# Optimization experiments

Measured on AMD Instinct MI355X. Metric: run time of the kernel, lower is better.

## Reference

```python
import jax, jax.numpy as jnp
import numpy as np

ALPHA = 0.2    # LeakyReLU negative slope (init arg alpha)
HEADS = 8
EPS = 1e-5     # LayerNorm eps


def setup_inputs() -> dict:
    key = jax.random.key(0)
    ks = jax.random.split(key, 16)
    B, S, D = 4, 1024, 256
    dh = D // HEADS  # 32
    x = jax.random.normal(ks[0], (B, S, D), jnp.float32)
    adj = (jax.random.uniform(ks[1], (B, S, S)) < 0.05).astype(jnp.float32)
    adj = jnp.maximum(adj, jnp.eye(S, dtype=jnp.float32)[None])

    def w(k, shape, fan):
        return jax.random.normal(k, shape, jnp.float32) * (fan ** -0.5)

    # GAT layer 0: in->hidden (concat heads)
    W0 = w(ks[2], (D, D), D); a_src0 = w(ks[3], (HEADS, dh), dh); a_dst0 = w(ks[4], (HEADS, dh), dh)
    # GAT layer 1: hidden->hidden (concat heads)
    W1 = w(ks[5], (D, D), D); a_src1 = w(ks[6], (HEADS, dh), dh); a_dst1 = w(ks[7], (HEADS, dh), dh)
    # GAT layer 2: hidden->out (mean over heads, head_dim = out_dim)
    W2 = w(ks[8], (D, HEADS * D), D); a_src2 = w(ks[9], (HEADS, D), D); a_dst2 = w(ks[10], (HEADS, D), D)
    # LayerNorm
    ln_g = jnp.ones((D,), jnp.float32); ln_b = jnp.zeros((D,), jnp.float32)
    # FFN: D -> 2D -> D
    ff_w1 = w(ks[11], (D, 2 * D), D); ff_b1 = jnp.zeros((2 * D,), jnp.float32)
    ff_w2 = w(ks[12], (2 * D, D), 2 * D); ff_b2 = jnp.zeros((D,), jnp.float32)
    return dict(adj=adj, x=x, W0=W0, a_src0=a_src0, a_dst0=a_dst0,
                W1=W1, a_src1=a_src1, a_dst1=a_dst1,
                W2=W2, a_src2=a_src2, a_dst2=a_dst2,
                ln_g=ln_g, ln_b=ln_b,
                ff_w1=ff_w1, ff_b1=ff_b1, ff_w2=ff_w2, ff_b2=ff_b2)


def _gat_layer(h, adj, W, a_src, a_dst, concat):
    B, S, _ = h.shape
    hp = jnp.einsum('bsi,io->bso', h, W).reshape(B, S, HEADS, -1)  # [B,S,H,dh]
    src = jnp.einsum('bshd,hd->bsh', hp, a_src)  # per-node source score
    dst = jnp.einsum('bshd,hd->bsh', hp, a_dst)  # per-node dest score
    # e[b,i,j,h] = LeakyReLU(src_i + dst_j), masked by adjacency
    e = jax.nn.leaky_relu(src[:, :, None, :] + dst[:, None, :, :], ALPHA)
    e = jnp.where(adj[..., None] > 0, e, jnp.float32(-1e9))
    attn = jax.nn.softmax(e, axis=2)  # softmax over neighbors j
    out = jnp.einsum('bijh,bjhd->bihd', attn, hp)
    return out.reshape(B, S, -1) if concat else out.mean(axis=2)


def reference(adj, x, W0, a_src0, a_dst0, W1, a_src1, a_dst1, W2, a_src2, a_dst2,
              ln_g, ln_b, ff_w1, ff_b1, ff_w2, ff_b2):
    # MultiAttentionGAT: 3 layers with residuals, ELU between layers
    h = jax.nn.elu(_gat_layer(x, adj, W0, a_src0, a_dst0, True) + x)
    h = jax.nn.elu(_gat_layer(h, adj, W1, a_src1, a_dst1, True) + h)
    h = _gat_layer(h, adj, W2, a_src2, a_dst2, False) + h
    # LayerNorm
    mu = h.mean(-1, keepdims=True)
    var = h.var(-1, keepdims=True)
    h = (h - mu) * jax.lax.rsqrt(var + EPS) * ln_g + ln_b
    # GELU FFN + residual
    ff = jnp.dot(jax.nn.gelu(jnp.dot(h, ff_w1) + ff_b1), ff_w2) + ff_b2
    return h + ff
```

## Files before the change

kernel.cpp:

```cpp
#include <hip/hip_runtime.h>
#include <hip/hip_bf16.h>

#define B_ 4
#define S_ 1024
#define D_ 256
#define H_ 8
#define LRELU_ALPHA 0.2f
#define MAXDEG 128

typedef __attribute__((ext_vector_type(8))) short short8;
typedef __attribute__((ext_vector_type(4))) float floatx4;

__device__ __forceinline__ float bf2f(unsigned short u) {
    union { unsigned int i; float f; } c; c.i = ((unsigned int)u) << 16; return c.f;
}
__device__ __forceinline__ unsigned short f2bf(float f) {
    union { float f; unsigned int u; } c; c.f = f;
    unsigned int r = (c.u + 0x7FFF + ((c.u >> 16) & 1)) >> 16;
    return (unsigned short)r;
}

__device__ void castT_body(const float* __restrict__ W, unsigned short* __restrict__ out,
                           int K, int N, int k0, int n0, float (*t)[33], int tid) {
    int tx = tid & 31, ty = tid >> 5;
#pragma unroll
    for (int i = 0; i < 4; ++i)
        t[ty + 8 * i][tx] = W[(size_t)(k0 + ty + 8 * i) * N + n0 + tx];
    __syncthreads();
#pragma unroll
    for (int i = 0; i < 4; ++i)
        out[(size_t)(n0 + ty + 8 * i) * K + k0 + tx] = f2bf(t[tx][ty + 8 * i]);
}

__global__ __launch_bounds__(256) void k_prep(
        const float* __restrict__ x, unsigned short* __restrict__ xb,
        const float* __restrict__ W0, unsigned short* __restrict__ W0t,
        const float* __restrict__ W1, unsigned short* __restrict__ W1t,
        const float* __restrict__ W2, unsigned short* __restrict__ W2t,
        const float* __restrict__ F1, unsigned short* __restrict__ F1t,
        const float* __restrict__ F2, unsigned short* __restrict__ F2t,
        const float* __restrict__ as2, const float* __restrict__ ad2,
        float* __restrict__ WS2, float* __restrict__ WD2,
        const float* __restrict__ adj, int* __restrict__ nbr, int* __restrict__ cnt) {
    __shared__ float t[32][33];
    __shared__ int c;
    int b = blockIdx.x, tid = threadIdx.x;
    if (b < 1024) {
        int i = b * 256 + tid;
        float4 v = ((const float4*)x)[i];
        ushort4 u; u.x = f2bf(v.x); u.y = f2bf(v.y); u.z = f2bf(v.z); u.w = f2bf(v.w);
        ((ushort4*)xb)[i] = u;
    } else if (b < 1088) {
        int i = b - 1024; castT_body(W0, W0t, 256, 256, (i & 7) * 32, (i >> 3) * 32, t, tid);
    } else if (b < 1152) {
        int i = b - 1088; castT_body(W1, W1t, 256, 256, (i & 7) * 32, (i >> 3) * 32, t, tid);
    } else if (b < 1664) {
        int i = b - 1152;
        int k0 = (i & 7) * 32, d0 = ((i >> 3) & 7) * 32, h = i >> 6;
        int tx = tid & 31, ty = tid >> 5;
#pragma unroll
        for (int q = 0; q < 4; ++q)
            t[ty + 8 * q][tx] = W2[(size_t)(k0 + ty + 8 * q) * 2048 + h * 256 + d0 + tx];
        __syncthreads();
#pragma unroll
        for (int q = 0; q < 4; ++q)
            W2t[(size_t)(d0 + ty + 8 * q) * 2048 + h * 256 + k0 + tx] = f2bf(t[tx][ty + 8 * q]);
    } else if (b < 1792) {
        int i = b - 1664; castT_body(F1, F1t, 256, 512, (i & 7) * 32, (i >> 3) * 32, t, tid);
    } else if (b < 1920) {
        int i = b - 1792; castT_body(F2, F2t, 512, 256, (i & 15) * 32, (i >> 4) * 32, t, tid);
    } else if (b < 2432) {
        int id = (b - 1920) * 4 + (tid >> 6);
        int h = id >> 8, k = id & 255;
        int lane = tid & 63;
        float4 w4 = *(const float4*)(W2 + (size_t)k * 2048 + h * 256 + lane * 4);
        float4 a4 = *(const float4*)(as2 + h * 256 + lane * 4);
        float4 d4 = *(const float4*)(ad2 + h * 256 + lane * 4);
        float s = w4.x * a4.x + w4.y * a4.y + w4.z * a4.z + w4.w * a4.w;
        float d = w4.x * d4.x + w4.y * d4.y + w4.z * d4.z + w4.w * d4.w;
#pragma unroll
        for (int o = 32; o; o >>= 1) { s += __shfl_xor(s, o); d += __shfl_xor(d, o); }
        if (lane == 0) { WS2[h * 256 + k] = s; WD2[h * 256 + k] = d; }
    } else {
        int row = b - 2432;
        if (tid == 0) c = 0;
        __syncthreads();
        float4 a4 = ((const float4*)(adj + (size_t)row * S_))[tid];
#pragma unroll
        for (int q = 0; q < 4; ++q) {
            float a = q == 0 ? a4.x : q == 1 ? a4.y : q == 2 ? a4.z : a4.w;
            if (a > 0.f) {
                int s = atomicAdd(&c, 1);
                if (s < MAXDEG) nbr[row * MAXDEG + s] = tid * 4 + q;
            }
        }
        __syncthreads();
        if (tid == 0) cnt[row] = c < MAXDEG ? c : MAXDEG;
    }
}

__global__ __launch_bounds__(256) void k_gemm_wide(const unsigned short* __restrict__ A,
        const unsigned short* __restrict__ Bt, float* __restrict__ P,
        int M, int N, int K, int Kc) {
    __shared__ unsigned short As[64][40];
    __shared__ unsigned short Bs[256][40];
    int tid = threadIdx.x;
    int bm = blockIdx.y * 64, bn = blockIdx.x * 256;
    int kbeg = blockIdx.z * Kc, kend = kbeg + Kc;
    int lane = tid & 63, wv = tid >> 6;
    int lrow = lane & 15, lq = lane >> 4;
    floatx4 acc[4][4] = {};
    int sm = tid >> 2, skq = (tid & 3) * 8;
    const unsigned short* Ap = A + (size_t)(bm + sm) * K + skq;
    const unsigned short* Bp0 = Bt + (size_t)(bn + sm) * K + skq;
    const unsigned short* Bp1 = Bp0 + (size_t)64 * K;
    const unsigned short* Bp2 = Bp0 + (size_t)128 * K;
    const unsigned short* Bp3 = Bp0 + (size_t)192 * K;
    short8 av  = *(const short8*)(Ap + kbeg);
    short8 bv0 = *(const short8*)(Bp0 + kbeg);
    short8 bv1 = *(const short8*)(Bp1 + kbeg);
    short8 bv2 = *(const short8*)(Bp2 + kbeg);
    short8 bv3 = *(const short8*)(Bp3 + kbeg);
    for (int k0 = kbeg; k0 < kend; k0 += 32) {
        *(short8*)&As[sm][skq]        = av;
        *(short8*)&Bs[sm][skq]        = bv0;
        *(short8*)&Bs[sm + 64][skq]   = bv1;
        *(short8*)&Bs[sm + 128][skq]  = bv2;
        *(short8*)&Bs[sm + 192][skq]  = bv3;
        __syncthreads();
        if (k0 + 32 < kend) {
            av  = *(const short8*)(Ap + k0 + 32);
            bv0 = *(const short8*)(Bp0 + k0 + 32);
            bv1 = *(const short8*)(Bp1 + k0 + 32);
            bv2 = *(const short8*)(Bp2 + k0 + 32);
            bv3 = *(const short8*)(Bp3 + k0 + 32);
        }
        short8 aF[4], bF[4];
#pragma unroll
        for (int mi = 0; mi < 4; ++mi)
            aF[mi] = *(const short8*)&As[mi * 16 + lrow][lq * 8];
#pragma unroll
        for (int ni = 0; ni < 4; ++ni)
            bF[ni] = *(const short8*)&Bs[wv * 64 + ni * 16 + lrow][lq * 8];
#pragma unroll
        for (int mi = 0; mi < 4; ++mi)
#pragma unroll
            for (int ni = 0; ni < 4; ++ni)
                acc[mi][ni] = __builtin_amdgcn_mfma_f32_16x16x32_bf16(aF[mi], bF[ni], acc[mi][ni], 0, 0, 0);
        __syncthreads();
    }
    float* out = P + (size_t)blockIdx.z * M * N;
#pragma unroll
    for (int mi = 0; mi < 4; ++mi)
#pragma unroll
        for (int ni = 0; ni < 4; ++ni)
#pragma unroll
            for (int r = 0; r < 4; ++r) {
                int grow = bm + mi * 16 + lq * 4 + r;
                int gcol = bn + wv * 64 + ni * 16 + lrow;
                out[(size_t)grow * N + gcol] = acc[mi][ni][r];
            }
}

template<int EPI>
__global__ __launch_bounds__(256) void k_gemm64(
        const unsigned short* __restrict__ A, const unsigned short* __restrict__ Bt,
        int N, int K,
        float* __restrict__ Pout, unsigned short* __restrict__ Ob,
        const float* __restrict__ p1, const float* __restrict__ p2,
        float* __restrict__ SRC, float* __restrict__ DST) {
    __shared__ unsigned short As[2][64][40];
    __shared__ unsigned short Bs[2][64][40];
    int tid = threadIdx.x;
    int bm = blockIdx.y * 64, bn = blockIdx.x * 64;
    int lane = tid & 63, wv = tid >> 6;
    int lrow = lane & 15, lq = lane >> 4;
    floatx4 acc[4] = {};
    int sm = tid >> 2, skq = (tid & 3) * 8;
    const unsigned short* Ap = A + (size_t)(bm + sm) * K + skq;
    const unsigned short* Bp = Bt + (size_t)(bn + sm) * K + skq;
    short8 av = *(const short8*)Ap;
    short8 bv = *(const short8*)Bp;
    *(short8*)&As[0][sm][skq] = av;
    *(short8*)&Bs[0][sm][skq] = bv;
    __syncthreads();
    int cur = 0;
    for (int k0 = 0; k0 < K; k0 += 32) {
        bool more = k0 + 32 < K;
        if (more) {
            av = *(const short8*)(Ap + k0 + 32);
            bv = *(const short8*)(Bp + k0 + 32);
        }
        short8 aF = *(const short8*)&As[cur][wv * 16 + lrow][lq * 8];
        short8 bF[4];
#pragma unroll
        for (int ni = 0; ni < 4; ++ni)
            bF[ni] = *(const short8*)&Bs[cur][ni * 16 + lrow][lq * 8];
#pragma unroll
        for (int ni = 0; ni < 4; ++ni)
            acc[ni] = __builtin_amdgcn_mfma_f32_16x16x32_bf16(aF, bF[ni], acc[ni], 0, 0, 0);
        if (more) {
            *(short8*)&As[cur ^ 1][sm][skq] = av;
            *(short8*)&Bs[cur ^ 1][sm][skq] = bv;
            __syncthreads();
            cur ^= 1;
        }
    }
    int row0 = bm + wv * 16 + lq * 4;
    if (EPI == 0) {
#pragma unroll
        for (int ni = 0; ni < 4; ++ni)
#pragma unroll
            for (int r = 0; r < 4; ++r)
                Ob[(size_t)(row0 + r) * N + bn + ni * 16 + lrow] = f2bf(acc[ni][r]);
        float asv[4], adv[4];
#pragma unroll
        for (int ni = 0; ni < 4; ++ni) {
            asv[ni] = p1[bn + ni * 16 + lrow];
            adv[ni] = p2[bn + ni * 16 + lrow];
        }
#pragma unroll
        for (int r = 0; r < 4; ++r) {
            float sA = acc[0][r] * asv[0] + acc[1][r] * asv[1];
            float sB = acc[2][r] * asv[2] + acc[3][r] * asv[3];
            float dA = acc[0][r] * adv[0] + acc[1][r] * adv[1];
            float dB = acc[2][r] * adv[2] + acc[3][r] * adv[3];
#pragma unroll
            for (int o = 8; o; o >>= 1) {
                sA += __shfl_xor(sA, o); sB += __shfl_xor(sB, o);
                dA += __shfl_xor(dA, o); dB += __shfl_xor(dB, o);
            }
            if (lrow == 0) {
                int h0 = bn >> 5;
                SRC[(row0 + r) * 8 + h0]     = sA;
                SRC[(row0 + r) * 8 + h0 + 1] = sB;
                DST[(row0 + r) * 8 + h0]     = dA;
                DST[(row0 + r) * 8 + h0 + 1] = dB;
            }
        }
    } else if (EPI == 2) {
#pragma unroll
        for (int ni = 0; ni < 4; ++ni) {
            int gcol = bn + ni * 16 + lrow;
            float bb = p1[gcol];
#pragma unroll
            for (int r = 0; r < 4; ++r) {
                float xx = acc[ni][r] + bb;
                float tt = tanhf(0.7978845608028654f * (xx + 0.044715f * xx * xx * xx));
                Ob[(size_t)(row0 + r) * N + gcol] = f2bf(0.5f * xx * (1.f + tt));
            }
        }
    } else if (EPI == 3) {
#pragma unroll
        for (int ni = 0; ni < 4; ++ni) {
            int gcol = bn + ni * 16 + lrow;
            float bb = p1[gcol];
#pragma unroll
            for (int r = 0; r < 4; ++r) {
                float res = p2[(size_t)(row0 + r) * 256 + gcol];
                Pout[(size_t)(row0 + r) * 256 + gcol] = acc[ni][r] + bb + res;
            }
        }
    }
}

__global__ __launch_bounds__(256) void k_attn4(const unsigned short* __restrict__ hp,
        const float* __restrict__ src, const float* __restrict__ dst,
        const int* __restrict__ nbr, const int* __restrict__ cnts,
        const float* __restrict__ X, float* __restrict__ Hout,
        unsigned short* __restrict__ Hb,
        const float* __restrict__ WS2, const float* __restrict__ WD2,
        float* __restrict__ SRC2, float* __restrict__ DST2) {
    int tid = threadIdx.x;
    int rq = tid >> 6;
    int lane = tid & 63;
    int row = blockIdx.x * 4 + rq;
    int rb = row & ~(S_ - 1);
    __shared__ int nb[4][MAXDEG];
    __shared__ float ew[4][MAXDEG * 9];
    int cnt = cnts[row];
    for (int t = lane; t < cnt; t += 64) nb[rq][t] = nbr[row * MAXDEG + t];
    float4 sa = *(const float4*)(src + row * H_);
    float4 sb = *(const float4*)(src + row * H_ + 4);
    for (int n = lane; n < cnt; n += 64) {
        int j = nb[rq][n];
        const float* dp = dst + (size_t)(rb + j) * H_;
        float4 da = *(const float4*)dp;
        float4 db = *(const float4*)(dp + 4);
        float e;
        e = sa.x + da.x; ew[rq][n * 9 + 0] = e > 0.f ? e : LRELU_ALPHA * e;
        e = sa.y + da.y; ew[rq][n * 9 + 1] = e > 0.f ? e : LRELU_ALPHA * e;
        e = sa.z + da.z; ew[rq][n * 9 + 2] = e > 0.f ? e : LRELU_ALPHA * e;
        e = sa.w + da.w; ew[rq][n * 9 + 3] = e > 0.f ? e : LRELU_ALPHA * e;
        e = sb.x + db.x; ew[rq][n * 9 + 4] = e > 0.f ? e : LRELU_ALPHA * e;
        e = sb.y + db.y; ew[rq][n * 9 + 5] = e > 0.f ? e : LRELU_ALPHA * e;
        e = sb.z + db.z; ew[rq][n * 9 + 6] = e > 0.f ? e : LRELU_ALPHA * e;
        e = sb.w + db.w; ew[rq][n * 9 + 7] = e > 0.f ? e : LRELU_ALPHA * e;
    }
    {
        int h = lane >> 3, s8 = lane & 7;
        float m = -1e30f;
        for (int n = s8; n < cnt; n += 8) m = fmaxf(m, ew[rq][n * 9 + h]);
#pragma unroll
        for (int o = 4; o; o >>= 1) m = fmaxf(m, __shfl_xor(m, o));
        float s = 0.f;
        for (int n = s8; n < cnt; n += 8) {
            float v = __expf(ew[rq][n * 9 + h] - m); ew[rq][n * 9 + h] = v; s += v;
        }
#pragma unroll
        for (int o = 4; o; o >>= 1) s += __shfl_xor(s, o);
        float inv = s > 0.f ? 1.f / s : 0.f;
        for (int n = s8; n < cnt; n += 8) ew[rq][n * 9 + h] *= inv;
    }
    int d0 = lane * 4;
    int h = lane >> 3;
    const unsigned short* hpb = hp + (size_t)rb * 256 + d0;
    const float* ewr = ew[rq];
    float A0 = 0.f, A1 = 0.f, A2 = 0.f, A3 = 0.f;
    float B0 = 0.f, B1 = 0.f, B2 = 0.f, B3 = 0.f;
    int n = 0;
    for (; n + 3 < cnt; n += 4) {
        int j0 = nb[rq][n], j1 = nb[rq][n + 1];
        int j2 = nb[rq][n + 2], j3 = nb[rq][n + 3];
        uint2 p0 = *(const uint2*)(hpb + (size_t)j0 * 256);
        uint2 p1 = *(const uint2*)(hpb + (size_t)j1 * 256);
        uint2 p2 = *(const uint2*)(hpb + (size_t)j2 * 256);
        uint2 p3 = *(const uint2*)(hpb + (size_t)j3 * 256);
        float w0 = ewr[n * 9 + h], w1 = ewr[(n + 1) * 9 + h];
        float w2 = ewr[(n + 2) * 9 + h], w3 = ewr[(n + 3) * 9 + h];
        A0 += w0 * bf2f((unsigned short)p0.x); A1 += w0 * bf2f((unsigned short)(p0.x >> 16));
        A2 += w0 * bf2f((unsigned short)p0.y); A3 += w0 * bf2f((unsigned short)(p0.y >> 16));
        B0 += w1 * bf2f((unsigned short)p1.x); B1 += w1 * bf2f((unsigned short)(p1.x >> 16));
        B2 += w1 * bf2f((unsigned short)p1.y); B3 += w1 * bf2f((unsigned short)(p1.y >> 16));
        A0 += w2 * bf2f((unsigned short)p2.x); A1 += w2 * bf2f((unsigned short)(p2.x >> 16));
        A2 += w2 * bf2f((unsigned short)p2.y); A3 += w2 * bf2f((unsigned short)(p2.y >> 16));
        B0 += w3 * bf2f((unsigned short)p3.x); B1 += w3 * bf2f((unsigned short)(p3.x >> 16));
        B2 += w3 * bf2f((unsigned short)p3.y); B3 += w3 * bf2f((unsigned short)(p3.y >> 16));
    }
    for (; n < cnt; ++n) {
        int j = nb[rq][n];
        uint2 p = *(const uint2*)(hpb + (size_t)j * 256);
        float w = ewr[n * 9 + h];
        A0 += w * bf2f((unsigned short)p.x); A1 += w * bf2f((unsigned short)(p.x >> 16));
        A2 += w * bf2f((unsigned short)p.y); A3 += w * bf2f((unsigned short)(p.y >> 16));
    }
    float4 xv = *(const float4*)(X + (size_t)row * 256 + d0);
    float ov0 = A0 + B0 + xv.x;
    float ov1 = A1 + B1 + xv.y;
    float ov2 = A2 + B2 + xv.z;
    float ov3 = A3 + B3 + xv.w;
    ov0 = ov0 > 0.f ? ov0 : (__expf(ov0) - 1.f);
    ov1 = ov1 > 0.f ? ov1 : (__expf(ov1) - 1.f);
    ov2 = ov2 > 0.f ? ov2 : (__expf(ov2) - 1.f);
    ov3 = ov3 > 0.f ? ov3 : (__expf(ov3) - 1.f);
    *(float4*)(Hout + (size_t)row * 256 + d0) = make_float4(ov0, ov1, ov2, ov3);
    ushort4 ub; ub.x = f2bf(ov0); ub.y = f2bf(ov1); ub.z = f2bf(ov2); ub.w = f2bf(ov3);
    *(ushort4*)(Hb + (size_t)row * 256 + d0) = ub;
    if (WS2 != nullptr) {
#pragma unroll
        for (int hh = 0; hh < 8; ++hh) {
            float4 wsv = *(const float4*)(WS2 + hh * 256 + d0);
            float4 wdv = *(const float4*)(WD2 + hh * 256 + d0);
            float sP = ov0 * wsv.x + ov1 * wsv.y + ov2 * wsv.z + ov3 * wsv.w;
            float dP = ov0 * wdv.x + ov1 * wdv.y + ov2 * wdv.z + ov3 * wdv.w;
#pragma unroll
            for (int o = 32; o; o >>= 1) { sP += __shfl_xor(sP, o); dP += __shfl_xor(dP, o); }
            if (lane == 0) { SRC2[row * 8 + hh] = sP; DST2[row * 8 + hh] = dP; }
        }
    }
}

__global__ __launch_bounds__(256) void k_attn_Y(const unsigned short* __restrict__ Hb,
        const float* __restrict__ src2, const float* __restrict__ dst2,
        const int* __restrict__ nbr, const int* __restrict__ cnts,
        unsigned short* __restrict__ Ycat) {
    int tid = threadIdx.x;
    int half = tid >> 7, sub = tid & 127;
    int row = blockIdx.x * 2 + half;
    int rb = row & ~(S_ - 1);
    __shared__ int nb[2][MAXDEG];
    __shared__ float ew[2][MAXDEG * 8];
    int cnt = cnts[row];
    for (int t = sub; t < cnt; t += 128) nb[half][t] = nbr[row * MAXDEG + t];
    float4 sa = *(const float4*)(src2 + row * H_);
    float4 sb = *(const float4*)(src2 + row * H_ + 4);
    __syncthreads();
    for (int n = sub; n < cnt; n += 128) {
        int j = nb[half][n];
        const float* dp = dst2 + (size_t)(rb + j) * H_;
        float4 da = *(const float4*)dp;
        float4 db = *(const float4*)(dp + 4);
        float e;
        e = sa.x + da.x; ew[half][n * 8 + 0] = e > 0.f ? e : LRELU_ALPHA * e;
        e = sa.y + da.y; ew[half][n * 8 + 1] = e > 0.f ? e : LRELU_ALPHA * e;
        e = sa.z + da.z; ew[half][n * 8 + 2] = e > 0.f ? e : LRELU_ALPHA * e;
        e = sa.w + da.w; ew[half][n * 8 + 3] = e > 0.f ? e : LRELU_ALPHA * e;
        e = sb.x + db.x; ew[half][n * 8 + 4] = e > 0.f ? e : LRELU_ALPHA * e;
        e = sb.y + db.y; ew[half][n * 8 + 5] = e > 0.f ? e : LRELU_ALPHA * e;
        e = sb.z + db.z; ew[half][n * 8 + 6] = e > 0.f ? e : LRELU_ALPHA * e;
        e = sb.w + db.w; ew[half][n * 8 + 7] = e > 0.f ? e : LRELU_ALPHA * e;
    }
    __syncthreads();
    {
        int h = sub >> 4, s16 = sub & 15;
        float m = -1e30f;
        for (int n = s16; n < cnt; n += 16) m = fmaxf(m, ew[half][n * 8 + h]);
#pragma unroll
        for (int o = 8; o; o >>= 1) m = fmaxf(m, __shfl_xor(m, o));
        float s = 0.f;
        for (int n = s16; n < cnt; n += 16) {
            float v = __expf(ew[half][n * 8 + h] - m); ew[half][n * 8 + h] = v; s += v;
        }
#pragma unroll
        for (int o = 8; o; o >>= 1) s += __shfl_xor(s, o);
        float inv = s > 0.f ? 0.125f / s : 0.f;
        for (int n = s16; n < cnt; n += 16) ew[half][n * 8 + h] *= inv;
    }
    __syncthreads();
    const unsigned short* hbase = Hb + (size_t)rb * 256 + 2 * sub;
    const float* ewh = ew[half];
    float aA[8] = {}, aB[8] = {};
    int n = 0;
    for (; n + 1 < cnt; n += 2) {
        int j0 = nb[half][n], j1 = nb[half][n + 1];
        unsigned int p0 = *(const unsigned int*)(hbase + (size_t)j0 * 256);
        unsigned int p1 = *(const unsigned int*)(hbase + (size_t)j1 * 256);
        float4 w0a = *(const float4*)(ewh + n * 8);
        float4 w0b = *(const float4*)(ewh + n * 8 + 4);
        float4 w1a = *(const float4*)(ewh + (n + 1) * 8);
        float4 w1b = *(const float4*)(ewh + (n + 1) * 8 + 4);
        float v0a = bf2f((unsigned short)p0), v0b = bf2f((unsigned short)(p0 >> 16));
        float v1a = bf2f((unsigned short)p1), v1b = bf2f((unsigned short)(p1 >> 16));
        aA[0] += w0a.x * v0a + w1a.x * v1a;  aB[0] += w0a.x * v0b + w1a.x * v1b;
        aA[1] += w0a.y * v0a + w1a.y * v1a;  aB[1] += w0a.y * v0b + w1a.y * v1b;
        aA[2] += w0a.z * v0a + w1a.z * v1a;  aB[2] += w0a.z * v0b + w1a.z * v1b;
        aA[3] += w0a.w * v0a + w1a.w * v1a;  aB[3] += w0a.w * v0b + w1a.w * v1b;
        aA[4] += w0b.x * v0a + w1b.x * v1a;  aB[4] += w0b.x * v0b + w1b.x * v1b;
        aA[5] += w0b.y * v0a + w1b.y * v1a;  aB[5] += w0b.y * v0b + w1b.y * v1b;
        aA[6] += w0b.z * v0a + w1b.z * v1a;  aB[6] += w0b.z * v0b + w1b.z * v1b;
        aA[7] += w0b.w * v0a + w1b.w * v1a;  aB[7] += w0b.w * v0b + w1b.w * v1b;
    }
    for (; n < cnt; ++n) {
        int j = nb[half][n];
        unsigned int p = *(const unsigned int*)(hbase + (size_t)j * 256);
        float4 wa = *(const float4*)(ewh + n * 8);
        float4 wb = *(const float4*)(ewh + n * 8 + 4);
        float va = bf2f((unsigned short)p), vb = bf2f((unsigned short)(p >> 16));
        aA[0] += wa.x * va; aB[0] += wa.x * vb;
        aA[1] += wa.y * va; aB[1] += wa.y * vb;
        aA[2] += wa.z * va; aB[2] += wa.z * vb;
        aA[3] += wa.w * va; aB[3] += wa.w * vb;
        aA[4] += wb.x * va; aB[4] += wb.x * vb;
        aA[5] += wb.y * va; aB[5] += wb.y * vb;
        aA[6] += wb.z * va; aB[6] += wb.z * vb;
        aA[7] += wb.w * va; aB[7] += wb.w * vb;
    }
    unsigned short* yb = Ycat + (size_t)row * 2048 + 2 * sub;
#pragma unroll
    for (int hh = 0; hh < 8; ++hh) {
        ushort2 u; u.x = f2bf(aA[hh]); u.y = f2bf(aB[hh]);
        *(ushort2*)(yb + hh * 256) = u;
    }
}

__global__ __launch_bounds__(256) void k_ln_red(const float* __restrict__ P, int nsplit,
        const float* __restrict__ Hres, const float* __restrict__ g,
        const float* __restrict__ bta, float* __restrict__ HLN,
        unsigned short* __restrict__ HLNb) {
    int row = blockIdx.x * 4 + (threadIdx.x >> 6);
    int lane = threadIdx.x & 63;
    float4 v = ((const float4*)(Hres + (size_t)row * 256))[lane];
    for (int sp = 0; sp < nsplit; ++sp) {
        float4 p = ((const float4*)(P + (size_t)sp * 1048576 + (size_t)row * 256))[lane];
        v.x += p.x; v.y += p.y; v.z += p.z; v.w += p.w;
    }
    float s = v.x + v.y + v.z + v.w;
    float q = v.x * v.x + v.y * v.y + v.z * v.z + v.w * v.w;
    for (int o = 32; o; o >>= 1) { s += __shfl_xor(s, o); q += __shfl_xor(q, o); }
    float mu = s * (1.f / 256.f);
    float var = q * (1.f / 256.f) - mu * mu;
    if (var < 0.f) var = 0.f;
    float rs = rsqrtf(var + 1e-5f);
    float4 gg = ((const float4*)g)[lane];
    float4 bb = ((const float4*)bta)[lane];
    float4 o;
    o.x = (v.x - mu) * rs * gg.x + bb.x;
    o.y = (v.y - mu) * rs * gg.y + bb.y;
    o.z = (v.z - mu) * rs * gg.z + bb.z;
    o.w = (v.w - mu) * rs * gg.w + bb.w;
    ((float4*)(HLN + (size_t)row * 256))[lane] = o;
    ushort4 ob; ob.x = f2bf(o.x); ob.y = f2bf(o.y); ob.z = f2bf(o.z); ob.w = f2bf(o.w);
    ((ushort4*)(HLNb + (size_t)row * 256))[lane] = ob;
}

extern "C" void kernel_launch(void* const* d_in, const int* in_sizes, int n_in,
                              void* d_out, int out_size, void* d_ws, size_t ws_size,
                              hipStream_t stream) {
    const float* adj   = (const float*)d_in[0];
    const float* x     = (const float*)d_in[1];
    const float* W0    = (const float*)d_in[2];
    const float* as0   = (const float*)d_in[3];
    const float* ad0   = (const float*)d_in[4];
    const float* W1    = (const float*)d_in[5];
    const float* as1   = (const float*)d_in[6];
    const float* ad1   = (const float*)d_in[7];
    const float* W2    = (const float*)d_in[8];
    const float* as2   = (const float*)d_in[9];
    const float* ad2   = (const float*)d_in[10];
    const float* ln_g  = (const float*)d_in[11];
    const float* ln_b  = (const float*)d_in[12];
    const float* ff_w1 = (const float*)d_in[13];
    const float* ff_b1 = (const float*)d_in[14];
    const float* ff_w2 = (const float*)d_in[15];
    const float* ff_b2 = (const float*)d_in[16];

    float* ws = (float*)d_ws;
    float* H    = ws;
    float* HLN  = ws + 1048576;
    unsigned short* Ycat = (unsigned short*)(ws + 2097152);
    unsigned short* HPb  = (unsigned short*)(ws + 6291456);
    unsigned short* xb   = (unsigned short*)(ws + 6815744);
    unsigned short* Hb   = (unsigned short*)(ws + 7340032);
    unsigned short* HLNb = (unsigned short*)(ws + 7864320);
    unsigned short* MIDb = (unsigned short*)(ws + 8388608);
    unsigned short* W0t  = (unsigned short*)(ws + 9437184);
    unsigned short* W1t  = (unsigned short*)(ws + 9469952);
    unsigned short* W2t  = (unsigned short*)(ws + 9502720);
    unsigned short* F1t  = (unsigned short*)(ws + 9764864);
    unsigned short* F2t  = (unsigned short*)(ws + 9830400);
    float* WS2  = ws + 9895936;
    float* WD2  = ws + 9897984;
    float* SRC  = ws + 9900032;
    float* DST  = ws + 9932800;
    float* SRC2 = ws + 9965568;
    float* DST2 = ws + 9998336;
    int*   NBR  = (int*)(ws + 10031104);
    int*   CNT  = (int*)(ws + 10555392);
    float* PP   = ws + 12582912;

    k_prep<<<6528, 256, 0, stream>>>(x, xb, W0, W0t, W1, W1t, W2, W2t,
                                     ff_w1, F1t, ff_w2, F2t, as2, ad2, WS2, WD2,
                                     adj, NBR, CNT);

    k_gemm64<0><<<dim3(4, 64), 256, 0, stream>>>(xb, W0t, 256, 256,
                                                 nullptr, HPb, as0, ad0, SRC, DST);
    k_attn4<<<1024, 256, 0, stream>>>(HPb, SRC, DST, NBR, CNT, x, H, Hb,
                                      nullptr, nullptr, nullptr, nullptr);

    k_gemm64<0><<<dim3(4, 64), 256, 0, stream>>>(Hb, W1t, 256, 256,
                                                 nullptr, HPb, as1, ad1, SRC, DST);
    k_attn4<<<1024, 256, 0, stream>>>(HPb, SRC, DST, NBR, CNT, H, H, Hb,
                                      WS2, WD2, SRC2, DST2);

    k_attn_Y<<<2048, 256, 0, stream>>>(Hb, SRC2, DST2, NBR, CNT, Ycat);
    k_gemm_wide<<<dim3(1, 64, 8), 256, 0, stream>>>(Ycat, W2t, PP, 4096, 256, 2048, 256);
    k_ln_red<<<1024, 256, 0, stream>>>(PP, 8, H, ln_g, ln_b, HLN, HLNb);

    k_gemm64<2><<<dim3(8, 64), 256, 0, stream>>>(HLNb, F1t, 512, 256,
                                                 nullptr, MIDb, ff_b1, nullptr, nullptr, nullptr);
    k_gemm64<3><<<dim3(4, 64), 256, 0, stream>>>(MIDb, F2t, 256, 512,
                                                 (float*)d_out, nullptr, ff_b2, HLN, nullptr, nullptr);
}
```

Measured before the change: 211.4 us.

## Fuse split-K reduction, LayerNorm and both FFN GEMMs into one tail kernel

Replaces the LayerNorm-reduction kernel and the two FFN GEMM launches with a single kernel. Each 512-thread block handles 16 rows: it sums the split-K partials, applies LayerNorm into shared memory, runs the first FFN GEMM with GELU into shared memory, then runs the second GEMM with bias and residual. This removes two launches and the global round trips for the normalised activations and the FFN intermediate. In exchange only 256 blocks run, each streams the full FFN weights from global/L2 with no double buffering, and every 32-wide k-step is guarded by two barriers.

```diff
diff --git a/kernel.cpp b/kernel.cpp
--- a/kernel.cpp
+++ b/kernel.cpp
@@ -162,11 +162,10 @@
             }
 }
 
-template<int EPI>
-__global__ __launch_bounds__(256) void k_gemm64(
+__global__ __launch_bounds__(256) void k_gemm64s(
         const unsigned short* __restrict__ A, const unsigned short* __restrict__ Bt,
         int N, int K,
-        float* __restrict__ Pout, unsigned short* __restrict__ Ob,
+        unsigned short* __restrict__ Ob,
         const float* __restrict__ p1, const float* __restrict__ p2,
         float* __restrict__ SRC, float* __restrict__ DST) {
     __shared__ unsigned short As[2][64][40];
@@ -207,59 +206,34 @@
         }
     }
     int row0 = bm + wv * 16 + lq * 4;
-    if (EPI == 0) {
-#pragma unroll
-        for (int ni = 0; ni < 4; ++ni)
-#pragma unroll
-            for (int r = 0; r < 4; ++r)
-                Ob[(size_t)(row0 + r) * N + bn + ni * 16 + lrow] = f2bf(acc[ni][r]);
-        float asv[4], adv[4];
-#pragma unroll
-        for (int ni = 0; ni < 4; ++ni) {
-            asv[ni] = p1[bn + ni * 16 + lrow];
-            adv[ni] = p2[bn + ni * 16 + lrow];
-        }
-#pragma unroll
-        for (int r = 0; r < 4; ++r) {
-            float sA = acc[0][r] * asv[0] + acc[1][r] * asv[1];
-            float sB = acc[2][r] * asv[2] + acc[3][r] * asv[3];
-            float dA = acc[0][r] * adv[0] + acc[1][r] * adv[1];
-            float dB = acc[2][r] * adv[2] + acc[3][r] * adv[3];
-#pragma unroll
-            for (int o = 8; o; o >>= 1) {
-                sA += __shfl_xor(sA, o); sB += __shfl_xor(sB, o);
-                dA += __shfl_xor(dA, o); dB += __shfl_xor(dB, o);
-            }
-            if (lrow == 0) {
-                int h0 = bn >> 5;
-                SRC[(row0 + r) * 8 + h0]     = sA;
-                SRC[(row0 + r) * 8 + h0 + 1] = sB;
-                DST[(row0 + r) * 8 + h0]     = dA;
-                DST[(row0 + r) * 8 + h0 + 1] = dB;
-            }
-        }
-    } else if (EPI == 2) {
-#pragma unroll
-        for (int ni = 0; ni < 4; ++ni) {
-            int gcol = bn + ni * 16 + lrow;
-            float bb = p1[gcol];
-#pragma unroll
-            for (int r = 0; r < 4; ++r) {
-                float xx = acc[ni][r] + bb;
-                float tt = tanhf(0.7978845608028654f * (xx + 0.044715f * xx * xx * xx));
-                Ob[(size_t)(row0 + r) * N + gcol] = f2bf(0.5f * xx * (1.f + tt));
-            }
-        }
-    } else if (EPI == 3) {
-#pragma unroll
-        for (int ni = 0; ni < 4; ++ni) {
-            int gcol = bn + ni * 16 + lrow;
-            float bb = p1[gcol];
-#pragma unroll
-            for (int r = 0; r < 4; ++r) {
-                float res = p2[(size_t)(row0 + r) * 256 + gcol];
-                Pout[(size_t)(row0 + r) * 256 + gcol] = acc[ni][r] + bb + res;
-            }
+#pragma unroll
+    for (int ni = 0; ni < 4; ++ni)
+#pragma unroll
+        for (int r = 0; r < 4; ++r)
+            Ob[(size_t)(row0 + r) * N + bn + ni * 16 + lrow] = f2bf(acc[ni][r]);
+    float asv[4], adv[4];
+#pragma unroll
+    for (int ni = 0; ni < 4; ++ni) {
+        asv[ni] = p1[bn + ni * 16 + lrow];
+        adv[ni] = p2[bn + ni * 16 + lrow];
+    }
+#pragma unroll
+    for (int r = 0; r < 4; ++r) {
+        float sA = acc[0][r] * asv[0] + acc[1][r] * asv[1];
+        float sB = acc[2][r] * asv[2] + acc[3][r] * asv[3];
+        float dA = acc[0][r] * adv[0] + acc[1][r] * adv[1];
+        float dB = acc[2][r] * adv[2] + acc[3][r] * adv[3];
+#pragma unroll
+        for (int o = 8; o; o >>= 1) {
+            sA += __shfl_xor(sA, o); sB += __shfl_xor(sB, o);
+            dA += __shfl_xor(dA, o); dB += __shfl_xor(dB, o);
+        }
+        if (lrow == 0) {
+            int h0 = bn >> 5;
+            SRC[(row0 + r) * 8 + h0]     = sA;
+            SRC[(row0 + r) * 8 + h0 + 1] = sB;
+            DST[(row0 + r) * 8 + h0]     = dA;
+            DST[(row0 + r) * 8 + h0 + 1] = dB;
         }
     }
 }
@@ -463,34 +437,108 @@
     }
 }
 
-__global__ __launch_bounds__(256) void k_ln_red(const float* __restrict__ P, int nsplit,
-        const float* __restrict__ Hres, const float* __restrict__ g,
-        const float* __restrict__ bta, float* __restrict__ HLN,
-        unsigned short* __restrict__ HLNb) {
-    int row = blockIdx.x * 4 + (threadIdx.x >> 6);
-    int lane = threadIdx.x & 63;
-    float4 v = ((const float4*)(Hres + (size_t)row * 256))[lane];
-    for (int sp = 0; sp < nsplit; ++sp) {
-        float4 p = ((const float4*)(P + (size_t)sp * 1048576 + (size_t)row * 256))[lane];
-        v.x += p.x; v.y += p.y; v.z += p.z; v.w += p.w;
-    }
-    float s = v.x + v.y + v.z + v.w;
-    float q = v.x * v.x + v.y * v.y + v.z * v.z + v.w * v.w;
-    for (int o = 32; o; o >>= 1) { s += __shfl_xor(s, o); q += __shfl_xor(q, o); }
-    float mu = s * (1.f / 256.f);
-    float var = q * (1.f / 256.f) - mu * mu;
-    if (var < 0.f) var = 0.f;
-    float rs = rsqrtf(var + 1e-5f);
+__global__ __launch_bounds__(512) void k_tail3(
+        const float* __restrict__ PP, const float* __restrict__ Hres,
+        const float* __restrict__ g, const float* __restrict__ bta,
+        const unsigned short* __restrict__ F1t, const float* __restrict__ b1,
+        const unsigned short* __restrict__ F2t, const float* __restrict__ b2,
+        float* __restrict__ out) {
+    __shared__ unsigned short alnb[16][264];
+    __shared__ float hln[16][260];
+    __shared__ unsigned short mid[16][520];
+    __shared__ unsigned short Bs[256][40];
+    int tid = threadIdx.x;
+    int lane = tid & 63, wv = tid >> 6;
+    int lrow = lane & 15, lq = lane >> 4;
+    int r0 = blockIdx.x * 16;
+
     float4 gg = ((const float4*)g)[lane];
-    float4 bb = ((const float4*)bta)[lane];
-    float4 o;
-    o.x = (v.x - mu) * rs * gg.x + bb.x;
-    o.y = (v.y - mu) * rs * gg.y + bb.y;
-    o.z = (v.z - mu) * rs * gg.z + bb.z;
-    o.w = (v.w - mu) * rs * gg.w + bb.w;
-    ((float4*)(HLN + (size_t)row * 256))[lane] = o;
-    ushort4 ob; ob.x = f2bf(o.x); ob.y = f2bf(o.y); ob.z = f2bf(o.z); ob.w = f2bf(o.w);
-    ((ushort4*)(HLNb + (size_t)row * 256))[lane] = ob;
+    float4 bbv = ((const float4*)bta)[lane];
+#pragma unroll
+    for (int pass = 0; pass < 2; ++pass) {
+        int lr = wv * 2 + pass;
+        int row = r0 + lr;
+        float4 v = ((const float4*)(Hres + (size_t)row * 256))[lane];
+#pragma unroll
+        for (int sp = 0; sp < 8; ++sp) {
+            float4 p = ((const float4*)(PP + (size_t)sp * 1048576 + (size_t)row * 256))[lane];
+            v.x += p.x; v.y += p.y; v.z += p.z; v.w += p.w;
+        }
+        float s = v.x + v.y + v.z + v.w;
+        float q = v.x * v.x + v.y * v.y + v.z * v.z + v.w * v.w;
+#pragma unroll
+        for (int o = 32; o; o >>= 1) { s += __shfl_xor(s, o); q += __shfl_xor(q, o); }
+        float mu = s * (1.f / 256.f);
+        float var = q * (1.f / 256.f) - mu * mu;
+        if (var < 0.f) var = 0.f;
+        float rs = rsqrtf(var + 1e-5f);
+        float4 o4;
+        o4.x = (v.x - mu) * rs * gg.x + bbv.x;
+        o4.y = (v.y - mu) * rs * gg.y + bbv.y;
+        o4.z = (v.z - mu) * rs * gg.z + bbv.z;
+        o4.w = (v.w - mu) * rs * gg.w + bbv.w;
+        *(float4*)&hln[lr][lane * 4] = o4;
+        ushort4 ub; ub.x = f2bf(o4.x); ub.y = f2bf(o4.y); ub.z = f2bf(o4.z); ub.w = f2bf(o4.w);
+        *(ushort4*)&alnb[lr][lane * 4] = ub;
+    }
+    __syncthreads();
+
+    int sm = tid >> 1, skq = (tid & 1) * 16;
+    int colb = wv * 32 + lrow;
+#pragma unroll 1
+    for (int hf = 0; hf < 2; ++hf) {
+        floatx4 acc1[2] = {};
+        const unsigned short* Fp = F1t + (size_t)(hf * 256 + sm) * 256 + skq;
+        for (int st = 0; st < 8; ++st) {
+            int k0 = st * 32;
+            *(short8*)&Bs[sm][skq]     = *(const short8*)(Fp + k0);
+            *(short8*)&Bs[sm][skq + 8] = *(const short8*)(Fp + k0 + 8);
+            __syncthreads();
+            short8 aF  = *(const short8*)&alnb[lrow][k0 + lq * 8];
+            short8 bF0 = *(const short8*)&Bs[wv * 32 + lrow][lq * 8];
+            short8 bF1 = *(const short8*)&Bs[wv * 32 + 16 + lrow][lq * 8];
+            acc1[0] = __builtin_amdgcn_mfma_f32_16x16x32_bf16(aF, bF0, acc1[0], 0, 0, 0);
+            acc1[1] = __builtin_amdgcn_mfma_f32_16x16x32_bf16(aF, bF1, acc1[1], 0, 0, 0);
+            __syncthreads();
+        }
+#pragma unroll
+        for (int ni = 0; ni < 2; ++ni) {
+            int gcol = hf * 256 + colb + ni * 16;
+            float bb = b1[gcol];
+#pragma unroll
+            for (int r = 0; r < 4; ++r) {
+                float xx = acc1[ni][r] + bb;
+                float tt = tanhf(0.7978845608028654f * (xx + 0.044715f * xx * xx * xx));
+                mid[lq * 4 + r][gcol] = f2bf(0.5f * xx * (1.f + tt));
+            }
+        }
+    }
+    __syncthreads();
+
+    floatx4 acc2[2] = {};
+    const unsigned short* F2p = F2t + (size_t)sm * 512 + skq;
+    for (int st = 0; st < 16; ++st) {
+        int k0 = st * 32;
+        *(short8*)&Bs[sm][skq]     = *(const short8*)(F2p + k0);
+        *(short8*)&Bs[sm][skq + 8] = *(const short8*)(F2p + k0 + 8);
+        __syncthreads();
+        short8 aF  = *(const short8*)&mid[lrow][k0 + lq * 8];
+        short8 bF0 = *(const short8*)&Bs[wv * 32 + lrow][lq * 8];
+        short8 bF1 = *(const short8*)&Bs[wv * 32 + 16 + lrow][lq * 8];
+        acc2[0] = __builtin_amdgcn_mfma_f32_16x16x32_bf16(aF, bF0, acc2[0], 0, 0, 0);
+        acc2[1] = __builtin_amdgcn_mfma_f32_16x16x32_bf16(aF, bF1, acc2[1], 0, 0, 0);
+        __syncthreads();
+    }
+#pragma unroll
+    for (int ni = 0; ni < 2; ++ni) {
+        int col = colb + ni * 16;
+        float bb = b2[col];
+#pragma unroll
+        for (int r = 0; r < 4; ++r) {
+            int lr = lq * 4 + r;
+            out[(size_t)(r0 + lr) * 256 + col] = acc2[ni][r] + bb + hln[lr][col];
+        }
+    }
 }
 
 extern "C" void kernel_launch(void* const* d_in, const int* in_sizes, int n_in,
@@ -516,13 +564,10 @@
 
     float* ws = (float*)d_ws;
     float* H    = ws;
-    float* HLN  = ws + 1048576;
     unsigned short* Ycat = (unsigned short*)(ws + 2097152);
     unsigned short* HPb  = (unsigned short*)(ws + 6291456);
     unsigned short* xb   = (unsigned short*)(ws + 6815744);
     unsigned short* Hb   = (unsigned short*)(ws + 7340032);
-    unsigned short* HLNb = (unsigned short*)(ws + 7864320);
-    unsigned short* MIDb = (unsigned short*)(ws + 8388608);
     unsigned short* W0t  = (unsigned short*)(ws + 9437184);
     unsigned short* W1t  = (unsigned short*)(ws + 9469952);
     unsigned short* W2t  = (unsigned short*)(ws + 9502720);
@@ -542,22 +587,17 @@
                                      ff_w1, F1t, ff_w2, F2t, as2, ad2, WS2, WD2,
                                      adj, NBR, CNT);
 
-    k_gemm64<0><<<dim3(4, 64), 256, 0, stream>>>(xb, W0t, 256, 256,
-                                                 nullptr, HPb, as0, ad0, SRC, DST);
+    k_gemm64s<<<dim3(4, 64), 256, 0, stream>>>(xb, W0t, 256, 256, HPb, as0, ad0, SRC, DST);
     k_attn4<<<1024, 256, 0, stream>>>(HPb, SRC, DST, NBR, CNT, x, H, Hb,
                                       nullptr, nullptr, nullptr, nullptr);
 
-    k_gemm64<0><<<dim3(4, 64), 256, 0, stream>>>(Hb, W1t, 256, 256,
-                                                 nullptr, HPb, as1, ad1, SRC, DST);
+    k_gemm64s<<<dim3(4, 64), 256, 0, stream>>>(Hb, W1t, 256, 256, HPb, as1, ad1, SRC, DST);
     k_attn4<<<1024, 256, 0, stream>>>(HPb, SRC, DST, NBR, CNT, H, H, Hb,
                                       WS2, WD2, SRC2, DST2);
 
     k_attn_Y<<<2048, 256, 0, stream>>>(Hb, SRC2, DST2, NBR, CNT, Ycat);
     k_gemm_wide<<<dim3(1, 64, 8), 256, 0, stream>>>(Ycat, W2t, PP, 4096, 256, 2048, 256);
-    k_ln_red<<<1024, 256, 0, stream>>>(PP, 8, H, ln_g, ln_b, HLN, HLNb);
-
-    k_gemm64<2><<<dim3(8, 64), 256, 0, stream>>>(HLNb, F1t, 512, 256,
-                                                 nullptr, MIDb, ff_b1, nullptr, nullptr, nullptr);
-    k_gemm64<3><<<dim3(4, 64), 256, 0, stream>>>(MIDb, F2t, 256, 512,
-                                                 (float*)d_out, nullptr, ff_b2, HLN, nullptr, nullptr);
-}
+
+    k_tail3<<<256, 512, 0, stream>>>(PP, H, ln_g, ln_b, F1t, ff_b1, F2t, ff_b2,
+                                     (float*)d_out);
+}
```

After: 212.0 us. About the same (+0.3%).
